# Kernel optimization log

Measured on AMD Instinct MI355X. Metric: run time of the kernel, lower is better.

Reference implementation:

```python
import jax, jax.numpy as jnp
import numpy as np
import math

B, S, E, H, F = 2, 2048, 1024, 16, 4096
D = E // H
EPS = 1e-5


def _layernorm(x, g, b):
    mu = jnp.mean(x, axis=-1, keepdims=True)
    var = jnp.mean(jnp.square(x - mu), axis=-1, keepdims=True)
    return (x - mu) * jax.lax.rsqrt(var + EPS) * g + b


def _xavier(k, fan_in, fan_out):
    limit = math.sqrt(6.0 / (fan_in + fan_out))
    return jax.random.uniform(k, (fan_in, fan_out), jnp.float32, -limit, limit)


def setup_inputs() -> dict:
    key = jax.random.key(0)
    ks = jax.random.split(key, 8)
    x = jax.random.normal(ks[0], (B, S, E), jnp.float32)
    # causal mask: 1 where attendable, 0 where masked (masked_fill at mask==0)
    mask = jnp.tril(jnp.ones((S, S), jnp.int32))[None, None]  # [1,1,S,S]
    return {
        "x": x,
        "mask": mask,
        "Wq": _xavier(ks[1], E, E), "bq": jnp.zeros((E,), jnp.float32),
        "Wk": _xavier(ks[2], E, E), "bk": jnp.zeros((E,), jnp.float32),
        "Wv": _xavier(ks[3], E, E), "bv": jnp.zeros((E,), jnp.float32),
        "Wo": _xavier(ks[4], E, E), "bo": jnp.zeros((E,), jnp.float32),
        "W1": _xavier(ks[5], E, F), "b1": jnp.zeros((F,), jnp.float32),
        "W2": _xavier(ks[6], F, E), "b2": jnp.zeros((E,), jnp.float32),
        "ln1_g": jnp.ones((E,), jnp.float32), "ln1_b": jnp.zeros((E,), jnp.float32),
        "ln2_g": jnp.ones((E,), jnp.float32), "ln2_b": jnp.zeros((E,), jnp.float32),
    }


def reference(x, mask, Wq, bq, Wk, bk, Wv, bv, Wo, bo, W1, b1, W2, b2,
              ln1_g, ln1_b, ln2_g, ln2_b):
    n = _layernorm(x, ln1_g, ln1_b)
    # project and split heads: [B,S,E] -> [B,H,S,D]
    def heads(w, b):
        return (n @ w + b).reshape(B, S, H, D).transpose(0, 2, 1, 3)
    Q, K, V = heads(Wq, bq), heads(Wk, bk), heads(Wv, bv)
    scores = jnp.einsum('bhsd,bhtd->bhst', Q, K) / math.sqrt(D)  # [B,H,S,S]
    scores = jnp.where(mask == 0, jnp.float32(-1e9), scores)
    attn = jax.nn.softmax(scores, axis=-1)
    ctx = jnp.einsum('bhst,bhtd->bhsd', attn, V)
    ctx = ctx.transpose(0, 2, 1, 3).reshape(B, S, E)
    attn_out = ctx @ Wo + bo
    x = _layernorm(x + attn_out, ln2_g, ln2_b)
    ffn = jax.nn.gelu(x @ W1 + b1, approximate=False) @ W2 + b2
    return x + ffn
```

## Files before the change

kernel.cpp:

```cpp
#include <hip/hip_runtime.h>
#include <cmath>

typedef unsigned short u16;
typedef unsigned int u32;
typedef __bf16 bf16x8 __attribute__((ext_vector_type(8)));
typedef float f32x4 __attribute__((ext_vector_type(4)));

#define SEQ 2048
#define EMB 1024
#define NHEAD 16
#define HDIM 64
#define FFDIM 4096
#define NBATCH 2
#define QKVLD 3072
#define PWS 68

#define QSCALE 0.18033688011112042f

__device__ __forceinline__ u16 f2bf(float f) {
  u32 u = __float_as_uint(f);
  u32 r = u + 0x7fffu + ((u >> 16) & 1u);
  return (u16)(r >> 16);
}

__device__ __forceinline__ float ex2(float x) {
#if __has_builtin(__builtin_amdgcn_exp2f)
  return __builtin_amdgcn_exp2f(x);
#else
  return exp2f(x);
#endif
}

__device__ __forceinline__ float geluf(float x) {
  float u = 0.7978845608028654f * (x + 0.044715f * x * x * x);
  float e = ex2(2.8853900817779268f * u);
  return x - x / (e + 1.0f);
}

__device__ __forceinline__ void gload16(const void* g, void* l) {
  __builtin_amdgcn_global_load_lds(
      (const __attribute__((address_space(1))) unsigned int*)g,
      (__attribute__((address_space(3))) unsigned int*)l, 16, 0, 0);
}

__device__ __forceinline__ u32 lds_addr(const void* p) {
  return (u32)(size_t)(const __attribute__((address_space(3))) void*)p;
}

template <int IMM>
__device__ __forceinline__ bf16x8 dsr16(u32 a) {
  bf16x8 r;
  asm volatile("ds_read_b128 %0, %1 offset:%2" : "=v"(r) : "v"(a), "n"(IMM));
  return r;
}

__device__ __forceinline__ void xcd_swizzle(int gx, int gy, int& bx, int& by) {
  int nwg = gx * gy;
  int lin = blockIdx.x + gx * blockIdx.y;
  int q = nwg >> 3;
  int nl = (lin & 7) * q + (lin >> 3);
  bx = nl % gx;
  by = nl / gx;
}

__global__ __launch_bounds__(256)
void wtrans_kernel(const float* __restrict__ W, u16* __restrict__ WT, int K, int N) {
  __shared__ float tile[32][33];
  int tx = threadIdx.x & 31, ty = threadIdx.x >> 5;
  int n0 = blockIdx.x * 32, k0 = blockIdx.y * 32;
#pragma unroll
  for (int i = 0; i < 32; i += 8)
    tile[ty + i][tx] = W[(size_t)(k0 + ty + i) * N + (n0 + tx)];
  __syncthreads();
#pragma unroll
  for (int i = 0; i < 32; i += 8)
    WT[(size_t)(n0 + ty + i) * K + (k0 + tx)] = f2bf(tile[tx][ty + i]);
}

__global__ __launch_bounds__(256)
void wtrans4_kernel(const float* __restrict__ W0, const float* __restrict__ W1_,
                    const float* __restrict__ W2_, const float* __restrict__ W3,
                    u16* __restrict__ Dqkv, u16* __restrict__ Do) {
  __shared__ float tile[32][33];
  int z = blockIdx.z;
  const float* W = (z == 0) ? W0 : (z == 1) ? W1_ : (z == 2) ? W2_ : W3;
  u16* D = (z < 3) ? (Dqkv + (size_t)z * EMB * EMB) : Do;
  int tx = threadIdx.x & 31, ty = threadIdx.x >> 5;
  int n0 = blockIdx.x * 32, k0 = blockIdx.y * 32;
#pragma unroll
  for (int i = 0; i < 32; i += 8)
    tile[ty + i][tx] = W[(size_t)(k0 + ty + i) * EMB + (n0 + tx)];
  __syncthreads();
#pragma unroll
  for (int i = 0; i < 32; i += 8)
    D[(size_t)(n0 + ty + i) * EMB + (k0 + tx)] = f2bf(tile[tx][ty + i]);
}

__global__ __launch_bounds__(256)
void vtrans_kernel(const u16* __restrict__ QKV, u16* __restrict__ Vt) {
  __shared__ u16 tile[64 * 72];
  int bh = blockIdx.y, b = bh >> 4, h = bh & 15;
  int s0 = blockIdx.x * 64;
  const u16* src = QKV + (size_t)b * SEQ * QKVLD + 2048 + (size_t)h * HDIM;
  int tid = threadIdx.x;
#pragma unroll
  for (int cc = 0; cc < 2; ++cc) {
    int c = tid + cc * 256;
    int s = c >> 3, d0 = (c & 7) * 8;
    uint4 v = *(const uint4*)(src + (size_t)(s0 + s) * QKVLD + d0);
    *(uint4*)(&tile[s * 72 + d0]) = v;
  }
  __syncthreads();
  u16* dst = Vt + (size_t)bh * HDIM * SEQ;
#pragma unroll
  for (int cc = 0; cc < 2; ++cc) {
    int c = tid + cc * 256;
    int d = c >> 3, t0l = (c & 7) * 8;
    union { uint4 u; u16 s[8]; } ou;
#pragma unroll
    for (int j = 0; j < 8; ++j) ou.s[j] = tile[(t0l + j) * 72 + d];
    *(uint4*)(dst + (size_t)d * SEQ + s0 + t0l) = ou.u;
  }
}

__global__ __launch_bounds__(256)
void ln_kernel(const float* __restrict__ in, const float* __restrict__ gamma,
               const float* __restrict__ beta, u16* __restrict__ outb) {
  int w = threadIdx.x >> 6, lane = threadIdx.x & 63;
  int row = blockIdx.x * 4 + w;
  size_t base = (size_t)row * EMB;
  float4 v[4];
  float s = 0.f, q = 0.f;
#pragma unroll
  for (int j = 0; j < 4; ++j) {
    v[j] = *(const float4*)(in + base + j * 256 + lane * 4);
    s += v[j].x + v[j].y + v[j].z + v[j].w;
    q += v[j].x * v[j].x + v[j].y * v[j].y + v[j].z * v[j].z + v[j].w * v[j].w;
  }
#pragma unroll
  for (int off = 1; off < 64; off <<= 1) {
    s += __shfl_xor(s, off);
    q += __shfl_xor(q, off);
  }
  float mean = s * (1.0f / EMB);
  float var = q * (1.0f / EMB) - mean * mean;
  float rstd = rsqrtf(var + 1e-5f);
#pragma unroll
  for (int j = 0; j < 4; ++j) {
    int c = j * 256 + lane * 4;
    float4 g4 = *(const float4*)(gamma + c);
    float4 b4 = *(const float4*)(beta + c);
    ushort4 ob;
    ob.x = f2bf((v[j].x - mean) * rstd * g4.x + b4.x);
    ob.y = f2bf((v[j].y - mean) * rstd * g4.y + b4.y);
    ob.z = f2bf((v[j].z - mean) * rstd * g4.z + b4.z);
    ob.w = f2bf((v[j].w - mean) * rstd * g4.w + b4.w);
    *(ushort4*)(outb + base + c) = ob;
  }
}

__global__ __launch_bounds__(256)
void ln2f_kernel(const float* __restrict__ p, size_t pstride,
                 const float* __restrict__ bias, const float* __restrict__ resid,
                 const float* __restrict__ gamma, const float* __restrict__ beta,
                 u16* __restrict__ outb, float* __restrict__ outf) {
  int w = threadIdx.x >> 6, lane = threadIdx.x & 63;
  int row = blockIdx.x * 4 + w;
  size_t base = (size_t)row * EMB;
  float4 v[4];
  float s = 0.f, q = 0.f;
#pragma unroll
  for (int j = 0; j < 4; ++j) {
    int c = j * 256 + lane * 4;
    float4 a = *(const float4*)(p + base + c);
    float4 b = *(const float4*)(p + pstride + base + c);
    float4 r = *(const float4*)(resid + base + c);
    float4 bb = *(const float4*)(bias + c);
    v[j].x = a.x + b.x + r.x + bb.x;
    v[j].y = a.y + b.y + r.y + bb.y;
    v[j].z = a.z + b.z + r.z + bb.z;
    v[j].w = a.w + b.w + r.w + bb.w;
    s += v[j].x + v[j].y + v[j].z + v[j].w;
    q += v[j].x * v[j].x + v[j].y * v[j].y + v[j].z * v[j].z + v[j].w * v[j].w;
  }
#pragma unroll
  for (int off = 1; off < 64; off <<= 1) {
    s += __shfl_xor(s, off);
    q += __shfl_xor(q, off);
  }
  float mean = s * (1.0f / EMB);
  float var = q * (1.0f / EMB) - mean * mean;
  float rstd = rsqrtf(var + 1e-5f);
#pragma unroll
  for (int j = 0; j < 4; ++j) {
    int c = j * 256 + lane * 4;
    float4 g4 = *(const float4*)(gamma + c);
    float4 b4 = *(const float4*)(beta + c);
    float y0 = (v[j].x - mean) * rstd * g4.x + b4.x;
    float y1 = (v[j].y - mean) * rstd * g4.y + b4.y;
    float y2 = (v[j].z - mean) * rstd * g4.z + b4.z;
    float y3 = (v[j].w - mean) * rstd * g4.w + b4.w;
    ushort4 ob;
    ob.x = f2bf(y0); ob.y = f2bf(y1); ob.z = f2bf(y2); ob.w = f2bf(y3);
    *(ushort4*)(outb + base + c) = ob;
    *(float4*)(outf + base + c) = make_float4(y0, y1, y2, y3);
  }
}

__global__ __launch_bounds__(256)
void reduce2_kernel(const float* __restrict__ p, size_t pstride,
                    const float* __restrict__ bias, const float* __restrict__ resid,
                    float* __restrict__ out, int ncols) {
  size_t i = ((size_t)blockIdx.x * 256 + threadIdx.x) * 4;
  float4 a = *(const float4*)(p + i);
  float4 b = *(const float4*)(p + pstride + i);
  float4 r = *(const float4*)(resid + i);
  int col = (int)(i & (size_t)(ncols - 1));
  float4 bb = *(const float4*)(bias + col);
  float4 o;
  o.x = a.x + b.x + r.x + bb.x;
  o.y = a.y + b.y + r.y + bb.y;
  o.z = a.z + b.z + r.z + bb.z;
  o.w = a.w + b.w + r.w + bb.w;
  *(float4*)(out + i) = o;
}

__global__ __launch_bounds__(256)
void gemm_bt(const u16* __restrict__ A, const u16* __restrict__ BT,
             const float* __restrict__ bias, const float* __restrict__ bias2,
             const float* __restrict__ bias3, void* __restrict__ out,
             const float* __restrict__ resid, int M, int N, int K,
             int mode, float scale, int ksplit,
             float* __restrict__ partial, size_t pstride) {
  __shared__ __align__(16) u16 As[128 * 64];
  __shared__ __align__(16) u16 Bs[128 * 64];
  int tid = threadIdx.x;
  int lane = tid & 63, w = tid >> 6;
  int wm = w >> 1, wn = w & 1;
  int g = lane >> 4, lr = lane & 15;
  int bx, by;
  xcd_swizzle(gridDim.x, gridDim.y, bx, by);
  int m0 = by * 128, n0 = bx * 128;
  int z = blockIdx.z;
  int kbeg = z * ksplit, kend = kbeg + ksplit;

  f32x4 acc[4][4];
#pragma unroll
  for (int mt = 0; mt < 4; ++mt)
#pragma unroll
    for (int nt = 0; nt < 4; ++nt) {
      acc[mt][nt][0] = 0.f; acc[mt][nt][1] = 0.f;
      acc[mt][nt][2] = 0.f; acc[mt][nt][3] = 0.f;
    }

  size_t ao[4], bo_[4];
  int lo[4];
#pragma unroll
  for (int cc = 0; cc < 4; ++cc) {
    int c = tid + cc * 256;
    int row = c >> 3, slot = c & 7;
    int gc = slot ^ (row & 7);
    ao[cc] = (size_t)(m0 + row) * K + gc * 8;
    bo_[cc] = (size_t)(n0 + row) * K + gc * 8;
    lo[cc] = c * 8;
  }
  int swz[2];
#pragma unroll
  for (int kk = 0; kk < 2; ++kk) swz[kk] = ((kk * 4 + g) ^ (lr & 7)) * 8;

  for (int k0 = kbeg; k0 < kend; k0 += 64) {
    __syncthreads();
#pragma unroll
    for (int cc = 0; cc < 4; ++cc) gload16(A + ao[cc] + k0, As + lo[cc]);
#pragma unroll
    for (int cc = 0; cc < 4; ++cc) gload16(BT + bo_[cc] + k0, Bs + lo[cc]);
    __syncthreads();
#pragma unroll
    for (int kk = 0; kk < 2; ++kk) {
      bf16x8 af[4], bfr[4];
#pragma unroll
      for (int mt = 0; mt < 4; ++mt)
        af[mt] = *(const bf16x8*)(As + (wm * 64 + mt * 16 + lr) * 64 + swz[kk]);
#pragma unroll
      for (int nt = 0; nt < 4; ++nt)
        bfr[nt] = *(const bf16x8*)(Bs + (wn * 64 + nt * 16 + lr) * 64 + swz[kk]);
#pragma unroll
      for (int mt = 0; mt < 4; ++mt)
#pragma unroll
        for (int nt = 0; nt < 4; ++nt)
          acc[mt][nt] = __builtin_amdgcn_mfma_f32_16x16x32_bf16(af[mt], bfr[nt], acc[mt][nt], 0, 0, 0);
    }
  }

  float* pz = partial + (size_t)z * pstride;
#pragma unroll
  for (int mt = 0; mt < 4; ++mt) {
    int row = m0 + wm * 64 + mt * 16 + g * 4;
#pragma unroll
    for (int nt = 0; nt < 4; ++nt) {
      int col = n0 + wn * 64 + nt * 16 + lr;
      float bcol;
      if (mode == 3) {
        int which = col >> 10;
        const float* bp = (which == 0) ? bias : (which == 1) ? bias2 : bias3;
        bcol = bp[col & 1023];
      } else if (mode != 4) {
        bcol = bias[col];
      } else {
        bcol = 0.f;
      }
#pragma unroll
      for (int r = 0; r < 4; ++r) {
        float vacc = acc[mt][nt][r] + bcol;
        size_t idx = (size_t)(row + r) * N + col;
        if (mode == 0)      ((u16*)out)[idx] = f2bf(vacc * scale);
        else if (mode == 1) ((u16*)out)[idx] = f2bf(geluf(vacc));
        else if (mode == 2) ((float*)out)[idx] = vacc + resid[idx];
        else if (mode == 3) ((u16*)out)[idx] = f2bf(col < 1024 ? vacc * QSCALE : vacc);
        else                pz[idx] = vacc;
      }
    }
  }
}


#define BARM __builtin_amdgcn_s_barrier()
#define VMWS asm volatile("s_waitcnt vmcnt(%0)" ::"n"(4 + RA))
#define VMW0 asm volatile("s_waitcnt vmcnt(0)")
#define NOSTG ((void)0)
#define NOWT ((void)0)

#define STG_A(t, d, kh)                                                       \
  { _Pragma("unroll")                                                         \
    for (int j = 0; j < RA; ++j)                                              \
      gload16(A + (size_t)sgA[j] + kbeg + (t) * 64 + (kh) * 32,               \
              As + ((d) * 2 + (kh)) * ABUF + slA[j]); }

#define STG_B(t, d, kh)                                                       \
  { _Pragma("unroll")                                                         \
    for (int j = 0; j < 2; ++j)                                               \
      gload16(BT + (size_t)sgB[j] + kbeg + (t) * 64 + (kh) * 32,              \
              Bs + ((d) * 2 + (kh)) * 8192 + slB[j]); }

#define PHASE(d, kk, mh, STAGE, WAITC)                                        \
  {                                                                           \
    const u32 bA = bB + ((d) * 2 + (kk)) * 16384;                             \
    const u32 aA = aB + ((d) * 2 + (kk)) * (ABUF * 2);                        \
    if ((mh) == 0) {                                                          \
      bfr[0] = dsr16<0>(bA);                                                  \
      bfr[1] = dsr16<1024>(bA);                                               \
      bfr[2] = dsr16<2048>(bA);                                               \
      bfr[3] = dsr16<3072>(bA);                                               \
    }                                                                         \
    bf16x8 af[MT2];                                                           \
    af[0] = dsr16<(((mh) * MT2 + 0) * 1024)>(aA);                             \
    af[1] = dsr16<(((mh) * MT2 + 1) * 1024)>(aA);                             \
    if constexpr (MT2 > 2) {                                                  \
      af[2] = dsr16<(((mh) * MT2 + 2) * 1024)>(aA);                           \
      af[3] = dsr16<(((mh) * MT2 + 3) * 1024)>(aA);                           \
    }                                                                         \
    STAGE;                                                                    \
    BARM;                                                                     \
    asm volatile("s_waitcnt lgkmcnt(0)");                                     \
    __builtin_amdgcn_sched_barrier(0);                                        \
    __builtin_amdgcn_s_setprio(1);                                            \
    _Pragma("unroll")                                                         \
    for (int mi = 0; mi < MT2; ++mi)                                          \
      _Pragma("unroll")                                                       \
      for (int nt = 0; nt < 4; ++nt)                                          \
        acc[(mh) * MT2 + mi][nt] = __builtin_amdgcn_mfma_f32_16x16x32_bf16(   \
            af[mi], bfr[nt], acc[(mh) * MT2 + mi][nt], 0, 0, 0);              \
    __builtin_amdgcn_s_setprio(0);                                            \
    WAITC;                                                                    \
    BARM;                                                                     \
  }

#define GEMM_EPILOGUE                                                         \
  float* pz = partial + (size_t)z * pstride;                                  \
  _Pragma("unroll")                                                           \
  for (int mt = 0; mt < MT; ++mt) {                                           \
    int row = m0 + wm * (BM / 2) + mt * 16 + g * 4;                           \
    _Pragma("unroll")                                                         \
    for (int nt = 0; nt < 4; ++nt) {                                          \
      int col = n0 + wn * 64 + nt * 16 + lr;                                  \
      float bcol;                                                             \
      if (mode == 3) {                                                        \
        int which = col >> 10;                                                \
        const float* bp = (which == 0) ? bias : (which == 1) ? bias2 : bias3; \
        bcol = bp[col & 1023];                                                \
      } else if (mode != 4) {                                                 \
        bcol = bias[col];                                                     \
      } else {                                                                \
        bcol = 0.f;                                                           \
      }                                                                       \
      _Pragma("unroll")                                                       \
      for (int r = 0; r < 4; ++r) {                                           \
        float vacc = acc[mt][nt][r] + bcol;                                   \
        size_t idx = (size_t)(row + r) * N + col;                             \
        if (mode == 0)      ((u16*)out)[idx] = f2bf(vacc * scale);            \
        else if (mode == 1) ((u16*)out)[idx] = f2bf(geluf(vacc));             \
        else if (mode == 2) ((float*)out)[idx] = vacc + resid[idx];           \
        else if (mode == 3) ((u16*)out)[idx] = f2bf(col < 1024 ? vacc * QSCALE : vacc); \
        else                pz[idx] = vacc;                                   \
      }                                                                       \
    }                                                                         \
  }

#define GEMM_PRELUDE                                                          \
  constexpr int MT = BM / 32;                                                 \
  constexpr int MT2 = MT / 2;                                                 \
  constexpr int RA = BM / 128;                                                \
  constexpr int ABUF = BM * 32;                                               \
  __shared__ __align__(16) u16 As[4 * ABUF];                                  \
  __shared__ __align__(16) u16 Bs[4 * 8192];                                  \
  int tid = threadIdx.x;                                                      \
  int lane = tid & 63, w = tid >> 6;                                          \
  int wm = w >> 2, wn = w & 3;                                                \
  int g = lane >> 4, lr = lane & 15;                                          \
  int bx, by;                                                                 \
  xcd_swizzle(gridDim.x, gridDim.y, bx, by);                                  \
  int m0 = by * BM, n0 = bx * 256;                                            \
  int z = blockIdx.z;                                                         \
  size_t kbeg = (size_t)z * ksplit;                                           \
  int nk = ksplit >> 6;                                                       \
  int phys = ((lr & 1) * 4 + g) ^ ((lr >> 1) & 7);                            \
  int aoff = wm * (BM / 2) * 32 + (lr >> 1) * 64 + phys * 8;                  \
  int boff = wn * 2048 + (lr >> 1) * 64 + phys * 8;                           \
  const u32 aB = lds_addr(As) + 2 * aoff;                                     \
  const u32 bB = lds_addr(Bs) + 2 * boff;                                     \
  int sgA[RA], slA[RA];                                                       \
  _Pragma("unroll")                                                           \
  for (int j = 0; j < RA; ++j) {                                              \
    int c = tid + j * 512;                                                    \
    int sr = c >> 3, ph = c & 7, l = ph ^ (sr & 7);                           \
    sgA[j] = (m0 + 2 * sr + (l >> 2)) * K + (l & 3) * 8;                      \
    slA[j] = c * 8;                                                           \
  }                                                                           \
  int sgB[2], slB[2];                                                         \
  _Pragma("unroll")                                                           \
  for (int j = 0; j < 2; ++j) {                                               \
    int c = tid + j * 512;                                                    \
    int sr = c >> 3, ph = c & 7, l = ph ^ (sr & 7);                           \
    sgB[j] = (n0 + 2 * sr + (l >> 2)) * K + (l & 3) * 8;                      \
    slB[j] = c * 8;                                                           \
  }                                                                           \
  f32x4 acc[MT][4];                                                           \
  _Pragma("unroll")                                                           \
  for (int mt = 0; mt < MT; ++mt)                                             \
    _Pragma("unroll")                                                         \
    for (int nt = 0; nt < 4; ++nt) {                                          \
      acc[mt][nt][0] = 0.f; acc[mt][nt][1] = 0.f;                             \
      acc[mt][nt][2] = 0.f; acc[mt][nt][3] = 0.f;                             \
    }                                                                         \
  bf16x8 bfr[4];

template <int BM>
__global__ __launch_bounds__(512, 2)
void gemm8(const u16* __restrict__ A, const u16* __restrict__ BT,
           const float* __restrict__ bias, const float* __restrict__ bias2,
           const float* __restrict__ bias3, void* __restrict__ out,
           const float* __restrict__ resid, int M, int N, int K,
           int mode, float scale, int ksplit,
           float* __restrict__ partial, size_t pstride) {
  GEMM_PRELUDE
  int npair = nk >> 1;

  STG_B(0, 0, 0); STG_A(0, 0, 0); STG_B(0, 0, 1); STG_A(0, 0, 1);
  STG_B(1, 1, 0); STG_A(1, 1, 0); STG_B(1, 1, 1);
  VMWS; BARM;

  for (int it = 0; it < npair - 1; ++it) {
    int t1 = 2 * it + 1, t2 = 2 * it + 2, t3 = 2 * it + 3;
    PHASE(0, 0, 0, STG_A(t1, 1, 1), NOWT)
    PHASE(0, 0, 1, STG_B(t2, 0, 0), NOWT)
    PHASE(0, 1, 0, STG_A(t2, 0, 0), NOWT)
    PHASE(0, 1, 1, STG_B(t2, 0, 1), VMWS)
    PHASE(1, 0, 0, STG_A(t2, 0, 1), NOWT)
    PHASE(1, 0, 1, STG_B(t3, 1, 0), NOWT)
    PHASE(1, 1, 0, STG_A(t3, 1, 0), NOWT)
    PHASE(1, 1, 1, STG_B(t3, 1, 1), VMWS)
  }
  {
    int t1 = nk - 1;
    PHASE(0, 0, 0, STG_A(t1, 1, 1), NOWT)
    PHASE(0, 0, 1, NOSTG, NOWT)
    PHASE(0, 1, 0, NOSTG, NOWT)
    PHASE(0, 1, 1, NOSTG, VMW0)
    PHASE(1, 0, 0, NOSTG, NOWT)
    PHASE(1, 0, 1, NOSTG, NOWT)
    PHASE(1, 1, 0, NOSTG, NOWT)
    PHASE(1, 1, 1, NOSTG, NOWT)
  }
  GEMM_EPILOGUE
}

__shared__ __align__(16) u16 attn_Kt[64 * 64];
__shared__ __align__(16) u16 attn_VT[64 * 64];
__shared__ __align__(16) u16 attn_Pw[2][4][16 * PWS];

template <int S0>
__device__ __forceinline__ void attn_tile(
    int t0, const int* q0, int w, int g, int lr, const bf16x8& ones,
    bf16x8 (&qf)[2][2], f32x4 (&lacc)[2], f32x4 (&oacc)[2][4]) {
  f32x4 sacc[2][4];
#pragma unroll
  for (int s = S0; s < 2; ++s)
#pragma unroll
    for (int nt = 0; nt < 4; ++nt) {
      sacc[s][nt][0] = 0.f; sacc[s][nt][1] = 0.f;
      sacc[s][nt][2] = 0.f; sacc[s][nt][3] = 0.f;
    }
#pragma unroll
  for (int kk = 0; kk < 2; ++kk)
#pragma unroll
    for (int nt = 0; nt < 4; ++nt) {
      int sw = ((kk * 4 + g) ^ lr) & 7;
      bf16x8 bfr = *(const bf16x8*)(&attn_Kt[(nt * 16 + lr) * 64 + sw * 8]);
      if (S0 == 0)
        sacc[0][nt] = __builtin_amdgcn_mfma_f32_16x16x32_bf16(qf[0][kk], bfr, sacc[0][nt], 0, 0, 0);
      sacc[1][nt] = __builtin_amdgcn_mfma_f32_16x16x32_bf16(qf[1][kk], bfr, sacc[1][nt], 0, 0, 0);
    }

#pragma unroll
  for (int s = S0; s < 2; ++s) {
    bool diag = (t0 == q0[s]);
#pragma unroll
    for (int r = 0; r < 4; ++r) {
#pragma unroll
      for (int nt = 0; nt < 4; ++nt) {
        float pv = ex2(sacc[s][nt][r]);
        if (diag && (nt * 16 + lr > w * 16 + g * 4 + r)) pv = 0.f;
        attn_Pw[s][w][(g * 4 + r) * PWS + nt * 16 + lr] = f2bf(pv);
      }
    }
  }

#pragma unroll
  for (int kk = 0; kk < 2; ++kk) {
    bf16x8 pf0, pf1;
    if (S0 == 0) pf0 = *(const bf16x8*)(&attn_Pw[0][w][lr * PWS + kk * 32 + g * 8]);
    pf1 = *(const bf16x8*)(&attn_Pw[1][w][lr * PWS + kk * 32 + g * 8]);
#pragma unroll
    for (int nt = 0; nt < 4; ++nt) {
      int sw = ((kk * 4 + g) ^ lr) & 7;
      bf16x8 vf = *(const bf16x8*)(&attn_VT[(nt * 16 + lr) * 64 + sw * 8]);
      if (S0 == 0)
        oacc[0][nt] = __builtin_amdgcn_mfma_f32_16x16x32_bf16(pf0, vf, oacc[0][nt], 0, 0, 0);
      oacc[1][nt] = __builtin_amdgcn_mfma_f32_16x16x32_bf16(pf1, vf, oacc[1][nt], 0, 0, 0);
    }
    if (S0 == 0)
      lacc[0] = __builtin_amdgcn_mfma_f32_16x16x32_bf16(pf0, ones, lacc[0], 0, 0, 0);
    lacc[1] = __builtin_amdgcn_mfma_f32_16x16x32_bf16(pf1, ones, lacc[1], 0, 0, 0);
  }
}

__global__ __launch_bounds__(256)
void attn2_kernel(const u16* __restrict__ QKV, const u16* __restrict__ Vt,
                  u16* __restrict__ ctx) {
  int tid = threadIdx.x, lane = tid & 63, w = tid >> 6;
  int g = lane >> 4, lr = lane & 15;
  int bh = blockIdx.y, b = bh >> 4, h = bh & 15;
  int q0[2];
  q0[0] = blockIdx.x * 64;
  q0[1] = (SEQ / 64 - 1 - blockIdx.x) * 64;
  const u16* Qh = QKV + (size_t)b * SEQ * QKVLD + (size_t)h * HDIM;
  const u16* Kh = Qh + 1024;
  const u16* Vth = Vt + (size_t)bh * HDIM * SEQ;

  bf16x8 ones;
#pragma unroll
  for (int j = 0; j < 8; ++j) ones[j] = (__bf16)1.0f;

  bf16x8 qf[2][2];
#pragma unroll
  for (int s = 0; s < 2; ++s)
#pragma unroll
    for (int kk = 0; kk < 2; ++kk)
      qf[s][kk] = *(const bf16x8*)(Qh + (size_t)(q0[s] + w * 16 + lr) * QKVLD + kk * 32 + g * 8);

  f32x4 lacc[2];
  f32x4 oacc[2][4];
#pragma unroll
  for (int s = 0; s < 2; ++s) {
    lacc[s][0] = 0.f; lacc[s][1] = 0.f; lacc[s][2] = 0.f; lacc[s][3] = 0.f;
#pragma unroll
    for (int nt = 0; nt < 4; ++nt) {
      oacc[s][nt][0] = 0.f; oacc[s][nt][1] = 0.f;
      oacc[s][nt][2] = 0.f; oacc[s][nt][3] = 0.f;
    }
  }

  int c1 = tid, c2 = tid + 256;
  int t1 = c1 >> 3, ch1 = (c1 ^ t1) & 7;
  int t2 = c2 >> 3, ch2 = (c2 ^ t2) & 7;
  for (int t0 = 0; t0 <= q0[1]; t0 += 64) {
    __syncthreads();
    gload16(Kh + (size_t)(t0 + t1) * QKVLD + ch1 * 8, attn_Kt + c1 * 8);
    gload16(Kh + (size_t)(t0 + t2) * QKVLD + ch2 * 8, attn_Kt + c2 * 8);
    gload16(Vth + (size_t)t1 * SEQ + t0 + ch1 * 8, attn_VT + c1 * 8);
    gload16(Vth + (size_t)t2 * SEQ + t0 + ch2 * 8, attn_VT + c2 * 8);
    __syncthreads();

    if (t0 <= q0[0])
      attn_tile<0>(t0, q0, w, g, lr, ones, qf, lacc, oacc);
    else
      attn_tile<1>(t0, q0, w, g, lr, ones, qf, lacc, oacc);
  }

#pragma unroll
  for (int s = 0; s < 2; ++s) {
    int srow = q0[s] + w * 16 + g * 4;
    float inv[4];
#pragma unroll
    for (int r = 0; r < 4; ++r) inv[r] = 1.0f / lacc[s][r];
#pragma unroll
    for (int nt = 0; nt < 4; ++nt) {
      int col = h * HDIM + nt * 16 + lr;
#pragma unroll
      for (int r = 0; r < 4; ++r) {
        float o = oacc[s][nt][r] * inv[r];
        ctx[((size_t)b * SEQ + srow + r) * EMB + col] = f2bf(o);
      }
    }
  }
}

extern "C" void kernel_launch(void* const* d_in, const int* in_sizes, int n_in,
                              void* d_out, int out_size, void* d_ws, size_t ws_size,
                              hipStream_t stream) {
  const float* x    = (const float*)d_in[0];
  const float* Wq   = (const float*)d_in[2];
  const float* bq   = (const float*)d_in[3];
  const float* Wk   = (const float*)d_in[4];
  const float* bk   = (const float*)d_in[5];
  const float* Wv   = (const float*)d_in[6];
  const float* bv   = (const float*)d_in[7];
  const float* Wo   = (const float*)d_in[8];
  const float* bo   = (const float*)d_in[9];
  const float* W1   = (const float*)d_in[10];
  const float* b1   = (const float*)d_in[11];
  const float* W2   = (const float*)d_in[12];
  const float* b2   = (const float*)d_in[13];
  const float* ln1g = (const float*)d_in[14];
  const float* ln1b = (const float*)d_in[15];
  const float* ln2g = (const float*)d_in[16];
  const float* ln2b = (const float*)d_in[17];

  char* ws = (char*)d_ws;
  u16* WqkvT = (u16*)(ws + ((size_t)0 << 20));
  u16* WoT   = (u16*)(ws + ((size_t)6 << 20));
  u16* W1T   = (u16*)(ws + ((size_t)8 << 20));
  u16* W2T   = (u16*)(ws + ((size_t)16 << 20));
  u16* xb    = (u16*)(ws + ((size_t)24 << 20));
  u16* QKVb  = (u16*)(ws + ((size_t)32 << 20));
  u16* ctxb  = (u16*)(ws + ((size_t)56 << 20));
  float* x2f = (float*)(ws + ((size_t)48 << 20));
  u16* x2b   = xb;
  u16* VtG   = (u16*)(ws + ((size_t)64 << 20));
  float* pWo = (float*)(ws + ((size_t)64 << 20));
  u16* h1    = (u16*)(ws + ((size_t)64 << 20));
  float* pF2 = (float*)(ws + ((size_t)0 << 20));

  dim3 blk(256);
  dim3 blk512(512);
  const int M = NBATCH * SEQ;

  wtrans4_kernel<<<dim3(32, 32, 4), blk, 0, stream>>>(Wq, Wk, Wv, Wo, WqkvT, WoT);
  wtrans_kernel<<<dim3(128, 32), blk, 0, stream>>>(W1, W1T, EMB, FFDIM);
  wtrans_kernel<<<dim3(32, 128), blk, 0, stream>>>(W2, W2T, FFDIM, EMB);

  ln_kernel<<<M / 4, blk, 0, stream>>>(x, ln1g, ln1b, xb);

  gemm_bt<<<dim3(QKVLD / 128, M / 128), blk, 0, stream>>>(
      xb, WqkvT, bq, bk, bv, QKVb, nullptr, M, QKVLD, EMB, 3, 1.0f, EMB, nullptr, 0);

  vtrans_kernel<<<dim3(SEQ / 64, NBATCH * NHEAD), blk, 0, stream>>>(QKVb, VtG);

  attn2_kernel<<<dim3(SEQ / 128, NBATCH * NHEAD), blk, 0, stream>>>(QKVb, VtG, ctxb);

  gemm8<128><<<dim3(EMB / 256, M / 128, 2), blk512, 0, stream>>>(
      ctxb, WoT, nullptr, nullptr, nullptr, nullptr, nullptr, M, EMB, EMB, 4, 1.0f,
      EMB / 2, pWo, (size_t)4 << 20);

  ln2f_kernel<<<M / 4, blk, 0, stream>>>(pWo, (size_t)4 << 20, bo, x, ln2g, ln2b,
                                         x2b, x2f);

  gemm8<256><<<dim3(FFDIM / 256, M / 256), blk512, 0, stream>>>(
      x2b, W1T, b1, nullptr, nullptr, h1, nullptr, M, FFDIM, EMB, 1, 1.0f, EMB,
      nullptr, 0);

  gemm8<128><<<dim3(EMB / 256, M / 128, 2), blk512, 0, stream>>>(
      h1, W2T, nullptr, nullptr, nullptr, nullptr, nullptr, M, EMB, FFDIM, 4, 1.0f,
      FFDIM / 2, pF2, (size_t)8 << 20);
  reduce2_kernel<<<M * EMB / 1024, blk, 0, stream>>>(pF2, (size_t)8 << 20, b2, x2f,
                                                     (float*)d_out, EMB);
}
```

Measured before the change: 400.5 us.

## Double-buffer K/V tiles in attention kernel to overlap loads with MFMA

Attention K and V^T shared-memory tiles become double-buffered, and the next tile is issued via async global-to-LDS loads before the current tile is computed. Explicit vmcnt waits and raw s_barrier replace __syncthreads, so memory latency can overlap with compute. This doubles LDS use for the K/V tiles and depends on the vmcnt count matching the number of outstanding loads and on LDS-write visibility without lgkmcnt waits.

```diff
diff --git a/kernel.cpp b/kernel.cpp
--- a/kernel.cpp
+++ b/kernel.cpp
@@ -494,13 +494,14 @@
   GEMM_EPILOGUE
 }
 
-__shared__ __align__(16) u16 attn_Kt[64 * 64];
-__shared__ __align__(16) u16 attn_VT[64 * 64];
+__shared__ __align__(16) u16 attn_Kt[2][64 * 64];
+__shared__ __align__(16) u16 attn_VT[2][64 * 64];
 __shared__ __align__(16) u16 attn_Pw[2][4][16 * PWS];
 
 template <int S0>
 __device__ __forceinline__ void attn_tile(
     int t0, const int* q0, int w, int g, int lr, const bf16x8& ones,
+    const u16* __restrict__ Kt, const u16* __restrict__ VT,
     bf16x8 (&qf)[2][2], f32x4 (&lacc)[2], f32x4 (&oacc)[2][4]) {
   f32x4 sacc[2][4];
 #pragma unroll
@@ -515,7 +516,7 @@
 #pragma unroll
     for (int nt = 0; nt < 4; ++nt) {
       int sw = ((kk * 4 + g) ^ lr) & 7;
-      bf16x8 bfr = *(const bf16x8*)(&attn_Kt[(nt * 16 + lr) * 64 + sw * 8]);
+      bf16x8 bfr = *(const bf16x8*)(&Kt[(nt * 16 + lr) * 64 + sw * 8]);
       if (S0 == 0)
         sacc[0][nt] = __builtin_amdgcn_mfma_f32_16x16x32_bf16(qf[0][kk], bfr, sacc[0][nt], 0, 0, 0);
       sacc[1][nt] = __builtin_amdgcn_mfma_f32_16x16x32_bf16(qf[1][kk], bfr, sacc[1][nt], 0, 0, 0);
@@ -543,7 +544,7 @@
 #pragma unroll
     for (int nt = 0; nt < 4; ++nt) {
       int sw = ((kk * 4 + g) ^ lr) & 7;
-      bf16x8 vf = *(const bf16x8*)(&attn_VT[(nt * 16 + lr) * 64 + sw * 8]);
+      bf16x8 vf = *(const bf16x8*)(&VT[(nt * 16 + lr) * 64 + sw * 8]);
       if (S0 == 0)
         oacc[0][nt] = __builtin_amdgcn_mfma_f32_16x16x32_bf16(pf0, vf, oacc[0][nt], 0, 0, 0);
       oacc[1][nt] = __builtin_amdgcn_mfma_f32_16x16x32_bf16(pf1, vf, oacc[1][nt], 0, 0, 0);
@@ -593,18 +594,36 @@
   int c1 = tid, c2 = tid + 256;
   int t1 = c1 >> 3, ch1 = (c1 ^ t1) & 7;
   int t2 = c2 >> 3, ch2 = (c2 ^ t2) & 7;
-  for (int t0 = 0; t0 <= q0[1]; t0 += 64) {
-    __syncthreads();
-    gload16(Kh + (size_t)(t0 + t1) * QKVLD + ch1 * 8, attn_Kt + c1 * 8);
-    gload16(Kh + (size_t)(t0 + t2) * QKVLD + ch2 * 8, attn_Kt + c2 * 8);
-    gload16(Vth + (size_t)t1 * SEQ + t0 + ch1 * 8, attn_VT + c1 * 8);
-    gload16(Vth + (size_t)t2 * SEQ + t0 + ch2 * 8, attn_VT + c2 * 8);
-    __syncthreads();
+
+  auto stage = [&](int buf, int t0) {
+    u16* KtB = attn_Kt[buf];
+    u16* VTB = attn_VT[buf];
+    gload16(Kh + (size_t)(t0 + t1) * QKVLD + ch1 * 8, KtB + c1 * 8);
+    gload16(Kh + (size_t)(t0 + t2) * QKVLD + ch2 * 8, KtB + c2 * 8);
+    gload16(Vth + (size_t)t1 * SEQ + t0 + ch1 * 8, VTB + c1 * 8);
+    gload16(Vth + (size_t)t2 * SEQ + t0 + ch2 * 8, VTB + c2 * 8);
+  };
+
+  int niter = (q0[1] >> 6) + 1;
+  stage(0, 0);
+  int cur = 0;
+  for (int it = 0; it < niter; ++it) {
+    int t0 = it << 6;
+    if (it + 1 < niter) {
+      stage(cur ^ 1, t0 + 64);
+      asm volatile("s_waitcnt vmcnt(4)");
+    } else {
+      asm volatile("s_waitcnt vmcnt(0)");
+    }
+    __builtin_amdgcn_s_barrier();
 
     if (t0 <= q0[0])
-      attn_tile<0>(t0, q0, w, g, lr, ones, qf, lacc, oacc);
+      attn_tile<0>(t0, q0, w, g, lr, ones, attn_Kt[cur], attn_VT[cur], qf, lacc, oacc);
     else
-      attn_tile<1>(t0, q0, w, g, lr, ones, qf, lacc, oacc);
+      attn_tile<1>(t0, q0, w, g, lr, ones, attn_Kt[cur], attn_VT[cur], qf, lacc, oacc);
+
+    __builtin_amdgcn_s_barrier();
+    cur ^= 1;
   }
 
 #pragma unroll
```

New measurement: 414.2 us. +3.4%, slower.
